# Performance work log

Measured on AMD Instinct MI355X. Metric: run time of the kernel, lower is better.

## Reference

```python
import jax, jax.numpy as jnp
import numpy as np

B, N, D, H, O, A, L = 128, 100, 2048, 1024, 1600, 400, 2048


def _mlp(x, w1, b1, w2, b2, w3, b3):
    h = jax.nn.relu(x @ w1 + b1)
    h = jax.nn.relu(h @ w2 + b2)
    return jax.nn.softmax(h @ w3 + b3, axis=2)  # softmax over class dim (dim=2)


def setup_inputs() -> dict:
    key = jax.random.key(0)
    ks = jax.random.split(key, 18)

    def lin(kw, fan_in, fan_out):
        s = 1.0 / np.sqrt(fan_in)
        return jax.random.normal(kw, (fan_in, fan_out), jnp.float32) * s

    x = jax.random.normal(ks[0], (B, N, D), jnp.float32)
    num_descs = jax.random.randint(ks[1], (B,), 0, N, jnp.int32)
    label_img = jnp.sort(jax.random.randint(ks[2], (L,), 0, B, jnp.int32))
    obj_labels = jax.random.randint(ks[3], (L,), 0, O)
    att_labels = jax.random.randint(ks[4], (L,), 0, A)

    inp = dict(x=x, num_descs=num_descs, label_img=label_img,
               obj_labels=obj_labels, att_labels=att_labels,
               w1o=lin(ks[5], D, H), b1o=jnp.zeros((H,), jnp.float32),
               w2o=lin(ks[6], H, H), b2o=jnp.zeros((H,), jnp.float32),
               w3o=lin(ks[7], H, O), b3o=jnp.zeros((O,), jnp.float32),
               w1a=lin(ks[8], D, H), b1a=jnp.zeros((H,), jnp.float32),
               w2a=lin(ks[9], H, H), b2a=jnp.zeros((H,), jnp.float32),
               w3a=lin(ks[10], H, A), b3a=jnp.zeros((A,), jnp.float32))
    return inp


def reference(x, num_descs, label_img, obj_labels, att_labels,
              w1o, b1o, w2o, b2o, w3o, b3o,
              w1a, b1a, w2a, b2a, w3a, b3a):
    po = _mlp(x, w1o, b1o, w2o, b2o, w3o, b3o)  # [B, N, O]
    pa = _mlp(x, w1a, b1a, w2a, b2a, w3a, b3a)  # [B, N, A]

    rows = jnp.arange(po.shape[1])  # [N]
    # per-label gather of the prob column for its object/attribute class -> [L, N]
    p_obj = po[label_img[:, None], rows[None, :], obj_labels[:, None]]
    p_att = pa[label_img[:, None], rows[None, :], att_labels[:, None]]
    # ragged unpad (descs beyond num_descs[img] excluded from argmax)
    valid = rows[None, :] < num_descs[label_img][:, None]
    score = jnp.where(valid, p_obj * p_att, -jnp.inf)
    desc = jnp.argmax(score, axis=1)  # [L]

    obj_dists = po[label_img, desc, :]  # [L, O]
    att_dists = pa[label_img, desc, :]  # [L, A]
    return (obj_dists, att_dists)
```

## Files before the change

kernel.cpp:

```cpp
#include <hip/hip_runtime.h>
#include <hip/hip_bf16.h>
#include <math.h>

#define Bq 128
#define Nq 100
#define Dq 2048
#define Hq 1024
#define Oq 1600
#define Aq 400
#define Lq 2048
#define Mq (Bq * Nq)
#define OqP 1664
#define AqP 512

typedef __attribute__((ext_vector_type(8))) short bf16x8;
typedef __attribute__((ext_vector_type(16))) float f32x16;
typedef unsigned short ushort;


__device__ __forceinline__ void split1(float v, ushort& h, ushort& l) {
    __hip_bfloat16 bh = __float2bfloat16(v);
    float fh = __bfloat162float(bh);
    __hip_bfloat16 bl = __float2bfloat16(v - fh);
    h = __builtin_bit_cast(ushort, bh);
    l = __builtin_bit_cast(ushort, bl);
}

__device__ __forceinline__ void gl_lds16(const ushort* g, ushort* lds) {
    __builtin_amdgcn_global_load_lds(
        (const __attribute__((address_space(1))) unsigned int*)g,
        (__attribute__((address_space(3))) unsigned int*)lds,
        16, 0, 0);
}

__global__ void build_offsets(const int* __restrict__ num_descs,
                              int* __restrict__ off, int* __restrict__ mc,
                              int* __restrict__ rowmap)
{
    __shared__ int cnt[Bq];
    __shared__ int offs[Bq + 1];
    const int t = threadIdx.x;
    int nd = num_descs[t];
    nd = nd < 0 ? 0 : (nd > Nq ? Nq : nd);
    const int c = nd < 1 ? 1 : nd;
    cnt[t] = c;
    __syncthreads();
    if (t == 0) {
        int s = 0;
        for (int i = 0; i < Bq; i++) { offs[i] = s; s += cnt[i]; }
        offs[Bq] = s;
        mc[0] = s;
        mc[1] = (s + 127) & ~127;
        mc[2] = (s + 255) & ~(int)255;
    }
    __syncthreads();
    off[t] = offs[t];
    for (int i = t; i < Mq; i += Bq) rowmap[i] = -1;
    __syncthreads();
    const int o = offs[t];
    for (int n = 0; n < c; n++) rowmap[o + n] = t * Nq + n;
}

__global__ __launch_bounds__(256) void split_compact(const float* __restrict__ x,
                              const int* __restrict__ rowmap,
                              const int* __restrict__ mc,
                              ushort* __restrict__ hi, ushort* __restrict__ lo)
{
    const int KB = Dq / 16;
    const int nbc = Dq / 64;
    const int rt = blockIdx.x / nbc;
    const int bc = (blockIdx.x - rt * nbc) * 64;
    if (rt * 32 >= mc[2]) return;

    __shared__ float t[32][66];
    const int tid = threadIdx.x;
    {
        const int row = tid >> 3;
        const int coff = (tid & 7) * 8;
        const int crow = rt * 32 + row;
        const int orig = (crow < mc[0]) ? rowmap[crow] : -1;
        float v[8];
        if (orig < 0) {
#pragma unroll
            for (int e = 0; e < 8; e++) v[e] = 0.f;
        } else {
            const float* src = x + (size_t)orig * Dq + bc + coff;
            float4 v0 = *(const float4*)(src);
            float4 v1 = *(const float4*)(src + 4);
            v[0] = v0.x; v[1] = v0.y; v[2] = v0.z; v[3] = v0.w;
            v[4] = v1.x; v[5] = v1.y; v[6] = v1.z; v[7] = v1.w;
        }
#pragma unroll
        for (int e = 0; e < 8; e++) t[row][coff + e] = v[e];
    }
    __syncthreads();

    const int wave = tid >> 6;
    const int lane = tid & 63;
    const int r32 = lane & 31;
    const int cl = wave * 16 + (lane >> 5) * 8;
    ushort h[8], l[8];
#pragma unroll
    for (int e = 0; e < 8; e++) split1(t[r32][cl + e], h[e], l[e]);
    const size_t wid = (size_t)rt * KB + (bc >> 4) + wave;
    const size_t a = wid * 512 + (size_t)lane * 8;
    *(bf16x8*)(hi + a) = *(bf16x8*)h;
    *(bf16x8*)(lo + a) = *(bf16x8*)l;
}

struct TSeg { const float* W; ushort* Th; ushort* Tl; int K; int N; int gx; int base; };
struct TSegs { TSeg s[6]; };

__global__ void tsplit_all(TSegs a)
{
    const int id = blockIdx.x;
    TSeg sg = a.s[5];
#pragma unroll
    for (int i = 4; i >= 0; i--) if (id < a.s[i + 1].base) sg = a.s[i];
    const int local = id - sg.base;
    const int bn = (local % sg.gx) * 32;
    const int bk = (local / sg.gx) * 32;
    const int KB = sg.K >> 4;

    __shared__ float t[32][33];
    const int tx = threadIdx.x & 31, ty = threadIdx.x >> 5;
#pragma unroll
    for (int i = 0; i < 4; i++) {
        const int k = bk + ty + i * 8, n = bn + tx;
        t[ty + i * 8][tx] = (n < sg.N) ? sg.W[(size_t)k * sg.N + n] : 0.f;
    }
    __syncthreads();

    const int wave = threadIdx.x >> 6;
    const int lane = threadIdx.x & 63;
    const int kc = wave & 1;
    const int hl = wave >> 1;
    const int nloc = lane & 31;
    const int kloc = kc * 16 + (lane >> 5) * 8;
    ushort v8[8];
#pragma unroll
    for (int e = 0; e < 8; e++) {
        ushort h, l;
        split1(t[kloc + e][nloc], h, l);
        v8[e] = hl ? l : h;
    }
    const size_t chunk = (size_t)((bn >> 5)) * KB + (bk >> 4) + kc;
    ushort* dst = (hl ? sg.Tl : sg.Th) + chunk * 512 + (size_t)lane * 8;
    *(bf16x8*)dst = *(bf16x8*)v8;
}

struct GArgs {
    const ushort* Ah; const ushort* Al;
    const ushort* Bh; const ushort* Bl;
    const float* bias;
    float* Cf; ushort* Ch; ushort* Cl;
    int K, Npad, Nreal, ldc, mode;
};

__global__ __launch_bounds__(256, 2) void gemm_split(GArgs g0, GArgs g1,
                                                     const int* __restrict__ mcp,
                                                     int nct0, int nct)
{
    const int ny = mcp[2] >> 8;
    const int nact = nct * ny;
    const int hw = blockIdx.x;
    if (hw >= nact) return;
    const int q = nact >> 3, r = nact & 7, xcd = hw & 7, pos = hw >> 3;
    const int L = (xcd < r ? xcd * (q + 1) : r * (q + 1) + (xcd - r) * q) + pos;
    const int by = L / nct;
    const int ct = L - by * nct;

    const GArgs g = (ct < nct0) ? g0 : g1;
    const int bm = by * 256;
    const int bn = (ct < nct0 ? ct : ct - nct0) * 128;

    const int KB = g.K >> 4;

    __shared__ __align__(16) ushort sAh[12288];
    __shared__ __align__(16) ushort sAl[12288];
    __shared__ __align__(16) ushort sBh[6144];
    __shared__ __align__(16) ushort sBl[6144];

    const int tid  = threadIdx.x;
    const int wave = tid >> 6;
    const int lane = tid & 63;
    const int wm = wave >> 1;
    const int wn = wave & 1;
    const int l31  = lane & 31;
    const int half = lane >> 5;

    const ushort* gAh0 = g.Ah + ((size_t)(bm / 32 + wave) * KB) * 512 + lane * 8;
    const ushort* gAh1 = g.Ah + ((size_t)(bm / 32 + wave + 4) * KB) * 512 + lane * 8;
    const ushort* gAl0 = g.Al + ((size_t)(bm / 32 + wave) * KB) * 512 + lane * 8;
    const ushort* gAl1 = g.Al + ((size_t)(bm / 32 + wave + 4) * KB) * 512 + lane * 8;
    const ushort* gBh  = g.Bh + ((size_t)(bn / 32 + wave) * KB) * 512 + lane * 8;
    const ushort* gBl  = g.Bl + ((size_t)(bn / 32 + wave) * KB) * 512 + lane * 8;

    f32x16 acc[4][2] = {};

    auto STAGE = [&](int c) {
        const size_t go = (size_t)c * 512;
        const int sa = (c % 3) * 4096;
        const int sb = (c % 3) * 2048;
        gl_lds16(gAh0 + go, &sAh[sa + (wave << 9)]);
        gl_lds16(gAh1 + go, &sAh[sa + ((wave + 4) << 9)]);
        gl_lds16(gAl0 + go, &sAl[sa + (wave << 9)]);
        gl_lds16(gAl1 + go, &sAl[sa + ((wave + 4) << 9)]);
        gl_lds16(gBh + go, &sBh[sb + (wave << 9)]);
        gl_lds16(gBl + go, &sBl[sb + (wave << 9)]);
    };

    auto PHASE = [&](int c, int stage_c, int drain) {
        const int sa = (c % 3) * 4096;
        const int sb = (c % 3) * 2048;
        bf16x8 ah[4], al[4], bh[2], bl[2];
#pragma unroll
        for (int i = 0; i < 4; i++) {
            const int o = sa + (wm * 4 + i) * 512 + lane * 8;
            ah[i] = *(const bf16x8*)&sAh[o];
            al[i] = *(const bf16x8*)&sAl[o];
        }
#pragma unroll
        for (int j = 0; j < 2; j++) {
            const int o = sb + (wn * 2 + j) * 512 + lane * 8;
            bh[j] = *(const bf16x8*)&sBh[o];
            bl[j] = *(const bf16x8*)&sBl[o];
        }
        if (stage_c >= 0) STAGE(stage_c);
        __builtin_amdgcn_s_setprio(1);
#pragma unroll
        for (int i = 0; i < 4; i++)
#pragma unroll
            for (int j = 0; j < 2; j++) {
                acc[i][j] = __builtin_amdgcn_mfma_f32_32x32x16_bf16(ah[i], bh[j], acc[i][j], 0, 0, 0);
                acc[i][j] = __builtin_amdgcn_mfma_f32_32x32x16_bf16(ah[i], bl[j], acc[i][j], 0, 0, 0);
                acc[i][j] = __builtin_amdgcn_mfma_f32_32x32x16_bf16(al[i], bh[j], acc[i][j], 0, 0, 0);
            }
        __builtin_amdgcn_s_setprio(0);
        if (drain == 6)      asm volatile("s_waitcnt vmcnt(6)" ::: "memory");
        else if (drain == 0) asm volatile("s_waitcnt vmcnt(0)" ::: "memory");
        if (drain >= 0) {
            asm volatile("s_waitcnt lgkmcnt(0)" ::: "memory");
            asm volatile("s_barrier" ::: "memory");
        }
    };

    STAGE(0); STAGE(1);
    asm volatile("s_waitcnt vmcnt(6)" ::: "memory");
    asm volatile("s_barrier" ::: "memory");

    for (int c = 0; c < KB - 2; ++c) PHASE(c, c + 2, 6);
    PHASE(KB - 2, -1, 0);
    PHASE(KB - 1, -1, -1);

    const int KC = g.ldc >> 4;
#pragma unroll
    for (int j = 0; j < 2; j++) {
        const int col = bn + (wn * 2 + j) * 32 + l31;
        if (col < g.Nreal) {
            const float bv = g.bias[col];
#pragma unroll
            for (int i = 0; i < 4; i++) {
#pragma unroll
                for (int r = 0; r < 16; r++) {
                    const int row = bm + (wm * 4 + i) * 32 + (r & 3) + 8 * (r >> 2) + 4 * half;
                    float v = acc[i][j][r] + bv;
                    if (g.mode == 1) {
                        v = fmaxf(v, 0.f);
                        ushort h, l;
                        split1(v, h, l);
                        const size_t chunk = (size_t)(row >> 5) * KC + (col >> 4);
                        const size_t adr = chunk * 512
                            + (size_t)((row & 31) + 32 * ((col >> 3) & 1)) * 8 + (col & 7);
                        g.Ch[adr] = h;
                        g.Cl[adr] = l;
                    } else {
                        g.Cf[(size_t)row * g.ldc + col] = v;
                    }
                }
            }
        }
    }
}

__global__ void softmax_stats2(const float* __restrict__ Zo, const float* __restrict__ Za,
                               const int* __restrict__ mc,
                               float* __restrict__ mxo, float* __restrict__ smo,
                               float* __restrict__ mxa, float* __restrict__ sma)
{
    const int r = blockIdx.x;
    if (r >= mc[0]) return;
    const float* Z; int ncols; float* mx; float* sm;
    if (blockIdx.y == 0) { Z = Zo; ncols = Oq; mx = mxo; sm = smo; }
    else                 { Z = Za; ncols = Aq; mx = mxa; sm = sma; }
    const float* row = Z + (size_t)r * ncols;
    __shared__ float red[256];
    float m = -INFINITY;
    for (int c = threadIdx.x; c < ncols; c += 256) m = fmaxf(m, row[c]);
    red[threadIdx.x] = m;
    __syncthreads();
    for (int s = 128; s > 0; s >>= 1) {
        if (threadIdx.x < s) red[threadIdx.x] = fmaxf(red[threadIdx.x], red[threadIdx.x + s]);
        __syncthreads();
    }
    m = red[0];
    __syncthreads();
    float su = 0.f;
    for (int c = threadIdx.x; c < ncols; c += 256) su += expf(row[c] - m);
    red[threadIdx.x] = su;
    __syncthreads();
    for (int s = 128; s > 0; s >>= 1) {
        if (threadIdx.x < s) red[threadIdx.x] += red[threadIdx.x + s];
        __syncthreads();
    }
    if (threadIdx.x == 0) { mx[r] = m; sm[r] = red[0]; }
}

__global__ void argmax_gather(
    const float* __restrict__ Zo, const float* __restrict__ Za,
    const float* __restrict__ mxo, const float* __restrict__ smo,
    const float* __restrict__ mxa, const float* __restrict__ sma,
    const int* __restrict__ label_img, const int* __restrict__ num_descs,
    const int* __restrict__ obj_labels, const int* __restrict__ att_labels,
    const int* __restrict__ off, float* __restrict__ out)
{
    const int l = blockIdx.x;
    const int b = label_img[l];
    const int nd = num_descs[b];
    const int r0 = off[b];
    const int t = threadIdx.x;

    __shared__ float ss[128];
    __shared__ int   si[128];
    if (t < 128) {
        float score = -INFINITY;
        if (t < Nq && t < nd) {
            const int r = r0 + t;
            const float po = expf(Zo[(size_t)r * Oq + obj_labels[l]] - mxo[r]) / smo[r];
            const float pa = expf(Za[(size_t)r * Aq + att_labels[l]] - mxa[r]) / sma[r];
            score = po * pa;
        }
        ss[t] = score;
        si[t] = t;
    }
    __syncthreads();
    for (int s = 64; s > 0; s >>= 1) {
        if (t < s) {
            const float s2 = ss[t + s];
            const int   i2 = si[t + s];
            if (s2 > ss[t] || (s2 == ss[t] && i2 < si[t])) { ss[t] = s2; si[t] = i2; }
        }
        __syncthreads();
    }
    const int r = r0 + si[0];

    const float mo = mxo[r], so = smo[r];
    const float* zo = Zo + (size_t)r * Oq;
    float* oo = out + (size_t)l * Oq;
    for (int c = t; c < Oq; c += 256)
        oo[c] = expf(zo[c] - mo) / so;

    const float ma = mxa[r], sa = sma[r];
    const float* za = Za + (size_t)r * Aq;
    float* oa = out + (size_t)Lq * Oq + (size_t)l * Aq;
    for (int c = t; c < Aq; c += 256)
        oa[c] = expf(za[c] - ma) / sa;
}

extern "C" void kernel_launch(void* const* d_in, const int* in_sizes, int n_in,
                              void* d_out, int out_size, void* d_ws, size_t ws_size,
                              hipStream_t stream)
{
    const float* x          = (const float*)d_in[0];
    const int*   num_descs  = (const int*)d_in[1];
    const int*   label_img  = (const int*)d_in[2];
    const int*   obj_labels = (const int*)d_in[3];
    const int*   att_labels = (const int*)d_in[4];
    const float* w1o = (const float*)d_in[5];  const float* b1o = (const float*)d_in[6];
    const float* w2o = (const float*)d_in[7];  const float* b2o = (const float*)d_in[8];
    const float* w3o = (const float*)d_in[9];  const float* b3o = (const float*)d_in[10];
    const float* w1a = (const float*)d_in[11]; const float* b1a = (const float*)d_in[12];
    const float* w2a = (const float*)d_in[13]; const float* b2a = (const float*)d_in[14];
    const float* w3a = (const float*)d_in[15]; const float* b3a = (const float*)d_in[16];
    float* out = (float*)d_out;

    char* p = (char*)d_ws;
    auto carve = [&](size_t bytes) { char* q = p; p += (bytes + 255) & ~(size_t)255; return q; };

    char* bufA = carve((size_t)Mq * Dq * 2 * 2);
    char* bufB = carve((size_t)Mq * Hq * 2 * 2 * 2);
    ushort* w1oth = (ushort*)carve((size_t)Hq * Dq * 2);  ushort* w1otl = (ushort*)carve((size_t)Hq * Dq * 2);
    ushort* w1ath = (ushort*)carve((size_t)Hq * Dq * 2);  ushort* w1atl = (ushort*)carve((size_t)Hq * Dq * 2);
    ushort* w2oth = (ushort*)carve((size_t)Hq * Hq * 2);  ushort* w2otl = (ushort*)carve((size_t)Hq * Hq * 2);
    ushort* w2ath = (ushort*)carve((size_t)Hq * Hq * 2);  ushort* w2atl = (ushort*)carve((size_t)Hq * Hq * 2);
    ushort* w3oth = (ushort*)carve((size_t)OqP * Hq * 2); ushort* w3otl = (ushort*)carve((size_t)OqP * Hq * 2);
    ushort* w3ath = (ushort*)carve((size_t)AqP * Hq * 2); ushort* w3atl = (ushort*)carve((size_t)AqP * Hq * 2);
    float* mxo = (float*)carve(Mq * 4); float* smo = (float*)carve(Mq * 4);
    float* mxa = (float*)carve(Mq * 4); float* sma = (float*)carve(Mq * 4);
    int* off    = (int*)carve(Bq * 4);
    int* mc     = (int*)carve(4 * 4);
    int* rowmap = (int*)carve(Mq * 4);

    ushort* xh = (ushort*)bufA;
    ushort* xl = xh + (size_t)Mq * Dq;
    ushort* h2oh = (ushort*)bufA;
    ushort* h2ol = h2oh + (size_t)Mq * Hq;
    ushort* h2ah = h2ol + (size_t)Mq * Hq;
    ushort* h2al = h2ah + (size_t)Mq * Hq;
    ushort* h1oh = (ushort*)bufB;
    ushort* h1ol = h1oh + (size_t)Mq * Hq;
    ushort* h1ah = h1ol + (size_t)Mq * Hq;
    ushort* h1al = h1ah + (size_t)Mq * Hq;
    float* z3o = (float*)bufB;
    float* z3a = z3o + (size_t)Mq * Oq;

    build_offsets<<<1, 128, 0, stream>>>(num_descs, off, mc, rowmap);
    split_compact<<<(Mq / 32) * (Dq / 64), 256, 0, stream>>>(x, rowmap, mc, xh, xl);

    {
        TSegs ts;
        int base = 0;
        auto seg = [&](const float* W, ushort* Th, ushort* Tl, int K, int N, int Npad) {
            TSeg s; s.W = W; s.Th = Th; s.Tl = Tl; s.K = K; s.N = N;
            s.gx = Npad / 32; s.base = base; base += (Npad / 32) * (K / 32); return s;
        };
        ts.s[0] = seg(w1o, w1oth, w1otl, Dq, Hq, Hq);
        ts.s[1] = seg(w1a, w1ath, w1atl, Dq, Hq, Hq);
        ts.s[2] = seg(w2o, w2oth, w2otl, Hq, Hq, Hq);
        ts.s[3] = seg(w2a, w2ath, w2atl, Hq, Hq, Hq);
        ts.s[4] = seg(w3o, w3oth, w3otl, Hq, Oq, OqP);
        ts.s[5] = seg(w3a, w3ath, w3atl, Hq, Aq, AqP);
        tsplit_all<<<base, 256, 0, stream>>>(ts);
    }

    {
        GArgs go = { xh, xl, w1oth, w1otl, b1o, nullptr, h1oh, h1ol, Dq, Hq, Hq, Hq, 1 };
        GArgs ga = { xh, xl, w1ath, w1atl, b1a, nullptr, h1ah, h1al, Dq, Hq, Hq, Hq, 1 };
        gemm_split<<<16 * (Mq / 256), 256, 0, stream>>>(go, ga, mc, 8, 16);
    }
    {
        GArgs go = { h1oh, h1ol, w2oth, w2otl, b2o, nullptr, h2oh, h2ol, Hq, Hq, Hq, Hq, 1 };
        GArgs ga = { h1ah, h1al, w2ath, w2atl, b2a, nullptr, h2ah, h2al, Hq, Hq, Hq, Hq, 1 };
        gemm_split<<<16 * (Mq / 256), 256, 0, stream>>>(go, ga, mc, 8, 16);
    }
    {
        GArgs go = { h2oh, h2ol, w3oth, w3otl, b3o, z3o, nullptr, nullptr, Hq, OqP, Oq, Oq, 0 };
        GArgs ga = { h2ah, h2al, w3ath, w3atl, b3a, z3a, nullptr, nullptr, Hq, AqP, Aq, Aq, 0 };
        gemm_split<<<(OqP / 128 + AqP / 128) * (Mq / 256), 256, 0, stream>>>(go, ga, mc,
                                                                            OqP / 128,
                                                                            OqP / 128 + AqP / 128);
    }

    softmax_stats2<<<dim3(Mq, 2), 256, 0, stream>>>(z3o, z3a, mc, mxo, smo, mxa, sma);
    argmax_gather<<<Lq, 256, 0, stream>>>(z3o, z3a, mxo, smo, mxa, sma,
                                          label_img, num_descs, obj_labels, att_labels, off, out);
}
```

Measured before the change: 546.8 us.

## Load high-part A fragments directly into registers, bypassing LDS

The high bf16 half of the A operand is now loaded from global memory straight into registers, one K-step ahead, using ping-pong register buffers. It is no longer staged through shared memory. This cuts LDS footprint and LDS read traffic and frees a shared buffer. In exchange, the two waves sharing each A row block both fetch it, so those global loads are duplicated. It also adds registers, unrolls the main loop by two, and retunes the vmcnt wait counts for the new load mix.

```diff
diff --git a/kernel.cpp b/kernel.cpp
--- a/kernel.cpp
+++ b/kernel.cpp
@@ -176,7 +176,6 @@
 
     const int KB = g.K >> 4;
 
-    __shared__ __align__(16) ushort sAh[12288];
     __shared__ __align__(16) ushort sAl[12288];
     __shared__ __align__(16) ushort sBh[6144];
     __shared__ __align__(16) ushort sBl[6144];
@@ -189,69 +188,78 @@
     const int l31  = lane & 31;
     const int half = lane >> 5;
 
-    const ushort* gAh0 = g.Ah + ((size_t)(bm / 32 + wave) * KB) * 512 + lane * 8;
-    const ushort* gAh1 = g.Ah + ((size_t)(bm / 32 + wave + 4) * KB) * 512 + lane * 8;
+    const ushort* pAh[4];
+#pragma unroll
+    for (int i = 0; i < 4; i++)
+        pAh[i] = g.Ah + ((size_t)(bm / 32 + wm * 4 + i) * KB) * 512 + lane * 8;
     const ushort* gAl0 = g.Al + ((size_t)(bm / 32 + wave) * KB) * 512 + lane * 8;
     const ushort* gAl1 = g.Al + ((size_t)(bm / 32 + wave + 4) * KB) * 512 + lane * 8;
     const ushort* gBh  = g.Bh + ((size_t)(bn / 32 + wave) * KB) * 512 + lane * 8;
     const ushort* gBl  = g.Bl + ((size_t)(bn / 32 + wave) * KB) * 512 + lane * 8;
 
     f32x16 acc[4][2] = {};
-
+    bf16x8 h0[4], h1[4];
+
+    auto LOADH = [&](int c, bf16x8 (&h)[4]) {
+#pragma unroll
+        for (int i = 0; i < 4; i++)
+            h[i] = *(const bf16x8*)(pAh[i] + (size_t)c * 512);
+    };
     auto STAGE = [&](int c) {
         const size_t go = (size_t)c * 512;
         const int sa = (c % 3) * 4096;
         const int sb = (c % 3) * 2048;
-        gl_lds16(gAh0 + go, &sAh[sa + (wave << 9)]);
-        gl_lds16(gAh1 + go, &sAh[sa + ((wave + 4) << 9)]);
         gl_lds16(gAl0 + go, &sAl[sa + (wave << 9)]);
         gl_lds16(gAl1 + go, &sAl[sa + ((wave + 4) << 9)]);
         gl_lds16(gBh + go, &sBh[sb + (wave << 9)]);
         gl_lds16(gBl + go, &sBl[sb + (wave << 9)]);
     };
 
-    auto PHASE = [&](int c, int stage_c, int drain) {
+    auto PHASE = [&](int c, bf16x8 (&hUse)[4], bf16x8 (&hNext)[4],
+                     int loadH, int stageC, int drain) {
         const int sa = (c % 3) * 4096;
         const int sb = (c % 3) * 2048;
-        bf16x8 ah[4], al[4], bh[2], bl[2];
-#pragma unroll
-        for (int i = 0; i < 4; i++) {
-            const int o = sa + (wm * 4 + i) * 512 + lane * 8;
-            ah[i] = *(const bf16x8*)&sAh[o];
-            al[i] = *(const bf16x8*)&sAl[o];
-        }
+        bf16x8 al[4], bh[2], bl[2];
+#pragma unroll
+        for (int i = 0; i < 4; i++)
+            al[i] = *(const bf16x8*)&sAl[sa + (wm * 4 + i) * 512 + lane * 8];
 #pragma unroll
         for (int j = 0; j < 2; j++) {
             const int o = sb + (wn * 2 + j) * 512 + lane * 8;
             bh[j] = *(const bf16x8*)&sBh[o];
             bl[j] = *(const bf16x8*)&sBl[o];
         }
-        if (stage_c >= 0) STAGE(stage_c);
+        if (stageC >= 0) STAGE(stageC);
+        if (loadH) LOADH(c + 1, hNext);
         __builtin_amdgcn_s_setprio(1);
 #pragma unroll
         for (int i = 0; i < 4; i++)
 #pragma unroll
             for (int j = 0; j < 2; j++) {
-                acc[i][j] = __builtin_amdgcn_mfma_f32_32x32x16_bf16(ah[i], bh[j], acc[i][j], 0, 0, 0);
-                acc[i][j] = __builtin_amdgcn_mfma_f32_32x32x16_bf16(ah[i], bl[j], acc[i][j], 0, 0, 0);
+                acc[i][j] = __builtin_amdgcn_mfma_f32_32x32x16_bf16(hUse[i], bh[j], acc[i][j], 0, 0, 0);
+                acc[i][j] = __builtin_amdgcn_mfma_f32_32x32x16_bf16(hUse[i], bl[j], acc[i][j], 0, 0, 0);
                 acc[i][j] = __builtin_amdgcn_mfma_f32_32x32x16_bf16(al[i], bh[j], acc[i][j], 0, 0, 0);
             }
         __builtin_amdgcn_s_setprio(0);
-        if (drain == 6)      asm volatile("s_waitcnt vmcnt(6)" ::: "memory");
-        else if (drain == 0) asm volatile("s_waitcnt vmcnt(0)" ::: "memory");
+        if (drain == 8)      asm volatile("s_waitcnt vmcnt(8)" ::: "memory");
+        else if (drain == 4) asm volatile("s_waitcnt vmcnt(4)" ::: "memory");
         if (drain >= 0) {
             asm volatile("s_waitcnt lgkmcnt(0)" ::: "memory");
             asm volatile("s_barrier" ::: "memory");
         }
     };
 
+    LOADH(0, h0);
     STAGE(0); STAGE(1);
-    asm volatile("s_waitcnt vmcnt(6)" ::: "memory");
+    asm volatile("s_waitcnt vmcnt(4)" ::: "memory");
     asm volatile("s_barrier" ::: "memory");
 
-    for (int c = 0; c < KB - 2; ++c) PHASE(c, c + 2, 6);
-    PHASE(KB - 2, -1, 0);
-    PHASE(KB - 1, -1, -1);
+    for (int c = 0; c < KB - 2; c += 2) {
+        PHASE(c,     h0, h1, 1, c + 2, 8);
+        PHASE(c + 1, h1, h0, 1, c + 3, 8);
+    }
+    PHASE(KB - 2, h0, h1, 1, -1, 4);
+    PHASE(KB - 1, h1, h0, 0, -1, -1);
 
     const int KC = g.ldc >> 4;
 #pragma unroll
```

Result: slower. 645.6 us (+18.1%).
